# Kernel optimization log

Measured on AMD Instinct MI355X. Metric: run time of the kernel, lower is better.

The kernel has to match this reference:

```python
import jax, jax.numpy as jnp
import numpy as np

# plan steps: (downsample_factor, bins_min, bins_max)
PLAN = [(2, 10, 14), (4, 16, 20)]


def _downsample(x, scale):
    # F.interpolate(mode='linear', align_corners=False, scale_factor=1/scale)
    in_len = x.shape[-1]
    out_len = in_len // scale
    sf = in_len / out_len
    src = jnp.maximum((jnp.arange(out_len, dtype=jnp.float32) + 0.5) * sf - 0.5, 0.0)
    i0 = jnp.floor(src).astype(jnp.int32)
    w = src - i0
    i1 = jnp.minimum(i0 + 1, in_len - 1)
    return x[..., i0] * (1.0 - w) + x[..., i1] * w


def _groupshiftadd(x, g):
    # one FFA butterfly stage with group size g
    B, C, R, nc = x.shape
    xg = x.reshape(B, C, R // g, g, nc)
    i = np.arange(g)
    iA = i // 2
    iB = iA + g // 2
    Bs = (i + 1) // 2
    # roll(v, Bs): y[j] = v[(j - Bs) mod nc]; static gather indices
    col = (np.arange(nc)[None, :] - Bs[:, None]) % nc  # (g, nc)
    a = xg[:, :, :, iA, :]                     # (B,C,G,g,nc)
    b = xg[:, :, :, iB[:, None], col]          # (B,C,G,g,nc) shifted rows
    return (a + b).reshape(B, C, R, nc)


def _forward(x):
    std_dev = jnp.std(x, axis=2, ddof=1)  # torch .std(2) is unbiased
    outs = []
    for ds, bmin, bmax in PLAN:
        down = _downsample(x, ds)
        L = down.shape[-1]
        for bins in range(bmin, bmax):
            trunc = L % bins
            arr = down[:, :, :L - trunc] if trunc else down
            r = arr.reshape(arr.shape[0], arr.shape[1], -1, bins)
            ini_rows = r.shape[2]
            k = int(np.ceil(np.log2(ini_rows)))
            target_rows = 2 ** k
            add = target_rows - ini_rows
            if add:
                pad = jnp.zeros((r.shape[0], r.shape[1], add, bins), r.dtype)
                r = jnp.concatenate([r, pad], axis=2)
            y = r
            for stage in range(1, k + 1):
                y = _groupshiftadd(y, 2 ** stage)
            mx = y.max(axis=3)
            # torch.median returns lower middle element for even sizes
            med = jnp.sort(y, axis=3)[..., (bins - 1) // 2]
            snr = (mx - med) / std_dev[:, :, None] / np.sqrt(float(ini_rows))
            outs.append(snr)  # (B, C, target_rows)
    return jnp.concatenate(outs, axis=2)


def setup_inputs() -> dict:
    key = jax.random.key(0)
    x = jax.random.normal(key, (8, 4, 262144), dtype=jnp.float32)
    return {"x": x}


def reference(x):
    return _forward(x)
```

## Files before the change

kernel.cpp:

```cpp
#include <hip/hip_runtime.h>
#include <cmath>


constexpr int NSEQ    = 32;
constexpr int NLEN    = 262144;
constexpr int OUTROWS = 81920;
constexpr int STDCH   = 32;

constexpr int cilog2(int v) { int r = 0; while (v > 1) { v >>= 1; ++r; } return r; }

constexpr size_t SCROFF[8] = {0, 6291456, 12582912, 18874368,
                              27262976, 29360128, 31981568, 34603008};

__device__ __forceinline__ unsigned bf16rne(float f) {
    unsigned u = __float_as_uint(f);
    return (u + 0x7FFFu + ((u >> 16) & 1u)) >> 16;
}
__device__ __forceinline__ unsigned pk2(float lo, float hi) {
    return bf16rne(lo) | (bf16rne(hi) << 16);
}

__global__ __launch_bounds__(256)
void std_partial(const float* __restrict__ x, float2* __restrict__ part)
{
    const int seq = blockIdx.x, ch = blockIdx.y;
    constexpr int N4 = NLEN / 4 / STDCH;
    const float4* xp = reinterpret_cast<const float4*>(x + (size_t)seq * NLEN) + (size_t)ch * N4;
    float s = 0.f, s2 = 0.f;
    for (int i = threadIdx.x; i < N4; i += 256) {
        float4 v = xp[i];
        s  += (v.x + v.y) + (v.z + v.w);
        s2 += (v.x * v.x + v.y * v.y) + (v.z * v.z + v.w * v.w);
    }
    #pragma unroll
    for (int off = 32; off > 0; off >>= 1) {
        s  += __shfl_down(s, off, 64);
        s2 += __shfl_down(s2, off, 64);
    }
    __shared__ float2 ws[4];
    const int w = threadIdx.x >> 6, l = threadIdx.x & 63;
    if (l == 0) ws[w] = make_float2(s, s2);
    __syncthreads();
    if (threadIdx.x == 0) {
        float a = ws[0].x + ws[1].x + ws[2].x + ws[3].x;
        float b = ws[0].y + ws[1].y + ws[2].y + ws[3].y;
        part[seq * STDCH + ch] = make_float2(a, b);
    }
}

template<int BINS, int G, int H1, int LP>
__device__ __forceinline__
void stageIP(float* __restrict__ buf, int s)
{
    constexpr int CST = G + 4;
    constexpr int PAIRS = G / 2;
    const int t = threadIdx.x;
    const int pr  = t & (PAIRS - 1);
    const int chi = t >> LP;
    const int c0  = chi * H1;
    const int half = 1 << (s - 1);
    const int qp = pr & (half - 1);
    const int grpbase = (pr >> (s - 1)) << s;
    const int rA = grpbase + qp, rB = rA + half, ro = grpbase + 2 * qp;
    const int shift = qp % BINS;

    float ra[H1], rb[H1 + 1];
    #pragma unroll
    for (int i = 0; i < H1; ++i) {
        int cc = c0 + i; if (cc >= BINS) cc = BINS - 1;
        ra[i] = buf[cc * CST + rA];
    }
    int idx = c0 - shift - 1; if (idx < 0) idx += BINS;
    #pragma unroll
    for (int i = 0; i < H1 + 1; ++i) {
        rb[i] = buf[idx * CST + rB];
        ++idx; if (idx == BINS) idx = 0;
    }
    __syncthreads();
    #pragma unroll
    for (int i = 0; i < H1; ++i) {
        const int c = c0 + i;
        if (c < BINS) {
            float2 o; o.x = ra[i] + rb[i + 1]; o.y = ra[i] + rb[i];
            *reinterpret_cast<float2*>(&buf[c * CST + ro]) = o;
        }
    }
    __syncthreads();
}

template<int DS, int BINS, int K, int S0, int CPAD>
__device__ __forceinline__
void passA_body(float* __restrict__ buf, const float* __restrict__ xs,
                unsigned short* __restrict__ scrC, int R, int blk, int sl)
{
    constexpr int G     = 1 << S0;
    constexpr int M     = 1 << (K - S0);
    constexpr int CST   = G + 4;
    constexpr int PAIRS = G / 2;
    constexpr int LP    = cilog2(PAIRS);
    constexpr int CS1   = 512 / PAIRS;
    constexpr int H1    = (BINS + CS1 - 1) / CS1;
    const int t = threadIdx.x;

    const int fmax = max(0, min(G * BINS, R * BINS - blk * G * BINS));

    if constexpr (DS == 2) {
        const float4* src4 = reinterpret_cast<const float4*>(xs + 2 * (size_t)blk * G * BINS);
        constexpr int NF4 = G * BINS / 2;
        for (int i = t; i < NF4; i += 512) {
            const int f0 = 2 * i;
            if (f0 < fmax) {
                float4 v = src4[i];
                int lr = f0 / BINS, c = f0 - lr * BINS;
                buf[c * CST + lr] = 0.5f * (v.x + v.y);
                if (f0 + 1 < fmax) {
                    int c1 = c + 1, lr1 = lr;
                    if (c1 == BINS) { c1 = 0; ++lr1; }
                    buf[c1 * CST + lr1] = 0.5f * (v.z + v.w);
                }
            }
        }
    } else {
        const float4* src4 = reinterpret_cast<const float4*>(xs + 4 * (size_t)blk * G * BINS);
        constexpr int NF4 = G * BINS;
        for (int i = t; i < NF4; i += 512) {
            if (i < fmax) {
                float4 v = src4[i];
                int lr = i / BINS, c = i - lr * BINS;
                buf[c * CST + lr] = 0.5f * (v.y + v.z);
            }
        }
    }
    for (int f = fmax + t; f < G * BINS; f += 512) {
        int lr = f / BINS, c = f - lr * BINS;
        buf[c * CST + lr] = 0.f;
    }
    __syncthreads();

    for (int s = 1; s <= S0; ++s)
        stageIP<BINS, G, H1, LP>(buf, s);

    const float* fin = buf;
    if constexpr (G == 512) {
        const int lr = t;
        unsigned u[CPAD / 2];
        #pragma unroll
        for (int k = 0; k < CPAD / 2; ++k) {
            const int ca = 2 * k, cbn = 2 * k + 1;
            float fa = (ca < BINS)  ? fin[ca * CST + lr]  : 0.f;
            float fb = (cbn < BINS) ? fin[cbn * CST + lr] : 0.f;
            u[k] = pk2(fa, fb);
        }
        unsigned short* dst = scrC + ((size_t)(sl * M + blk) * G + lr) * CPAD;
        if constexpr (CPAD == 12) {
            uint2* d2 = reinterpret_cast<uint2*>(dst);
            d2[0] = make_uint2(u[0], u[1]);
            d2[1] = make_uint2(u[2], u[3]);
            d2[2] = make_uint2(u[4], u[5]);
        } else {
            uint4* d4 = reinterpret_cast<uint4*>(dst);
            d4[0] = make_uint4(u[0], u[1], u[2], u[3]);
            d4[1] = make_uint4(u[4], u[5], u[6], u[7]);
        }
    } else {
        const int lr = t & 255, chh = t >> 8;
        constexpr int CH = CPAD / 2;
        unsigned u[CH / 2];
        #pragma unroll
        for (int k = 0; k < CH / 2; ++k) {
            const int ca = chh * CH + 2 * k, cbn = ca + 1;
            float fa = (ca < BINS)  ? fin[ca * CST + lr]  : 0.f;
            float fb = (cbn < BINS) ? fin[cbn * CST + lr] : 0.f;
            u[k] = pk2(fa, fb);
        }
        unsigned short* dst = scrC + ((size_t)(sl * M + blk) * G + lr) * CPAD + chh * CH;
        if constexpr (CH == 8) {
            *reinterpret_cast<uint4*>(dst) = make_uint4(u[0], u[1], u[2], u[3]);
        } else {
            unsigned* d = reinterpret_cast<unsigned*>(dst);
            #pragma unroll
            for (int k = 0; k < CH / 2; ++k) d[k] = u[k];
        }
    }
}

__global__ __launch_bounds__(512, 8)
void passA_all(const float* __restrict__ x, unsigned short* __restrict__ scr)
{
    __shared__ float buf[13 * 516];
    const int b = blockIdx.x;
    if (b < 4096) {
        const int cfg = b >> 10, r = b & 1023, blk = r & 31, sl = r >> 5;
        const float* xs = x + (size_t)sl * NLEN;
        switch (cfg) {
            case 0: passA_body<2, 10, 14, 9, 12>(buf, xs, scr + SCROFF[0], 13107, blk, sl); break;
            case 1: passA_body<2, 11, 14, 9, 12>(buf, xs, scr + SCROFF[1], 11915, blk, sl); break;
            case 2: passA_body<2, 12, 14, 9, 12>(buf, xs, scr + SCROFF[2], 10922, blk, sl); break;
            default: passA_body<2, 13, 14, 9, 16>(buf, xs, scr + SCROFF[3], 10082, blk, sl); break;
        }
    } else {
        const int b2 = b - 4096;
        const int cfg = b2 >> 9, r = b2 & 511, blk = r & 15, sl = r >> 4;
        const float* xs = x + (size_t)sl * NLEN;
        switch (cfg) {
            case 0: passA_body<4, 16, 12, 8, 16>(buf, xs, scr + SCROFF[4], 4096, blk, sl); break;
            case 1: passA_body<4, 17, 12, 8, 20>(buf, xs, scr + SCROFF[5], 3855, blk, sl); break;
            case 2: passA_body<4, 18, 12, 8, 20>(buf, xs, scr + SCROFF[6], 3640, blk, sl); break;
            default: passA_body<4, 19, 12, 8, 20>(buf, xs, scr + SCROFF[7], 3449, blk, sl); break;
        }
    }
}

template<int BINS, int M, int CST, int HB, int LQ>
__device__ __forceinline__
void fusedB(float* __restrict__ zpg, int s, int p, int sub)
{
    constexpr int QUADS = M / 4;
    const int Q   = sub & (QUADS - 1);
    const int chi = sub >> LQ;
    const int c0  = chi * HB;
    const int h = 1 << (s - 1), S = 1 << s;
    const int q  = Q & (h - 1);
    const int G2 = (Q >> (s - 1)) << (s + 1);
    const int rA0 = G2 + q, rA1 = rA0 + h, rB0 = G2 + S + q, rB1 = rB0 + h;
    const int vo = G2 + 4 * q;
    auto mbf = [](int x, int B) { int r = x % B; return r < 0 ? r + B : r; };
    const int ba1 = mbf(c0 - q - p * h - 1, BINS);
    const int bb0 = mbf(c0 - 2 * q - p * S - 2, BINS);
    const int bb1 = mbf(c0 - 3 * q - p * (S + h) - 3, BINS);

    float fa0[HB], fa1[HB + 1], fb0[HB + 2], fb1[HB + 3];
    #pragma unroll
    for (int i = 0; i < HB; ++i) {
        int cc = c0 + i; if (cc >= BINS) cc = BINS - 1;
        fa0[i] = zpg[cc * CST + rA0];
    }
    int idx = ba1;
    #pragma unroll
    for (int i = 0; i < HB + 1; ++i) {
        fa1[i] = zpg[idx * CST + rA1];
        ++idx; if (idx == BINS) idx = 0;
    }
    idx = bb0;
    #pragma unroll
    for (int i = 0; i < HB + 2; ++i) {
        fb0[i] = zpg[idx * CST + rB0];
        ++idx; if (idx == BINS) idx = 0;
    }
    idx = bb1;
    #pragma unroll
    for (int i = 0; i < HB + 3; ++i) {
        fb1[i] = zpg[idx * CST + rB1];
        ++idx; if (idx == BINS) idx = 0;
    }
    __syncthreads();
    #pragma unroll
    for (int i2 = 0; i2 < HB; ++i2) {
        const int c = c0 + i2;
        if (c < BINS) {
            float u0 = fa0[i2] + fa1[i2 + 1];
            float u1 = fa0[i2] + fa1[i2];
            float v0c  = fb0[i2 + 2] + fb1[i2 + 3];
            float v0p  = fb0[i2 + 1] + fb1[i2 + 2];
            float v1p  = fb0[i2 + 1] + fb1[i2 + 1];
            float v1pp = fb0[i2]     + fb1[i2];
            float4 o; o.x = u0 + v0c; o.y = u0 + v0p; o.z = u1 + v1p; o.w = u1 + v1pp;
            *reinterpret_cast<float4*>(&zpg[c * CST + vo]) = o;
        }
    }
    __syncthreads();
}

template<int BINS, int M, int CST, int HSB, int LP>
__device__ __forceinline__
void singleB(float* __restrict__ zpg, int s, int p, int sub)
{
    constexpr int PAIRSB = M / 2;
    const int pr  = sub & (PAIRSB - 1);
    const int chi = sub >> LP;
    const int c0  = chi * HSB;
    const int half = 1 << (s - 1);
    const int qp = pr & (half - 1);
    const int grpbase = (pr >> (s - 1)) << s;
    const int rA = grpbase + qp, rB = rA + half, ro = grpbase + 2 * qp;
    const int shift = (qp + p * half) % BINS;

    float ra[HSB], rb[HSB + 1];
    #pragma unroll
    for (int i = 0; i < HSB; ++i) {
        int cc = c0 + i; if (cc >= BINS) cc = BINS - 1;
        ra[i] = zpg[cc * CST + rA];
    }
    int idx = c0 - shift - 1;
    idx %= BINS; if (idx < 0) idx += BINS;
    #pragma unroll
    for (int i = 0; i < HSB + 1; ++i) {
        rb[i] = zpg[idx * CST + rB];
        ++idx; if (idx == BINS) idx = 0;
    }
    __syncthreads();
    #pragma unroll
    for (int i2 = 0; i2 < HSB; ++i2) {
        const int c = c0 + i2;
        if (c < BINS) {
            float2 o; o.x = ra[i2] + rb[i2 + 1]; o.y = ra[i2] + rb[i2];
            *reinterpret_cast<float2*>(&zpg[c * CST + ro]) = o;
        }
    }
    __syncthreads();
}

template<int BINS, int K, int S0, int CPAD, int OUTOFF>
__device__ __forceinline__
void passB_body(float* __restrict__ zb, float* __restrict__ s_red,
                const unsigned short* __restrict__ scrC, const float2* __restrict__ part,
                float* __restrict__ out, int R, int p_base, int sl)
{
    constexpr int G    = 1 << S0;
    constexpr int M    = 1 << (K - S0);
    constexpr int TS   = K - S0;
    constexpr int P    = 16;
    constexpr int CST  = M + 4;
    constexpr int BCST = BINS * CST;
    constexpr int LQB  = cilog2(M / 4);
    constexpr int CHB  = 32 / (M / 4);
    constexpr int HB   = (BINS + CHB - 1) / CHB;
    constexpr int LPB  = cilog2(M / 2);
    constexpr int CSB  = 32 / (M / 2);
    constexpr int HSB  = (BINS + CSB - 1) / CSB;

    const int t = threadIdx.x;

    if (t < 64) {
        float s = 0.f, s2 = 0.f;
        if (t < 32) { float2 pp = part[sl * STDCH + t]; s = pp.x; s2 = pp.y; }
        #pragma unroll
        for (int off = 16; off > 0; off >>= 1) {
            s  += __shfl_down(s, off, 64);
            s2 += __shfl_down(s2, off, 64);
        }
        if (t == 0) {
            const float n = (float)NLEN;
            s_red[0] = rsqrtf((s2 - s * s / n) / (n - 1.f)) * rsqrtf((float)R);
        }
    }

    {
        constexpr int RUN = P * CPAD / 4;
        constexpr int TOT = M * RUN;
        const unsigned short* base = scrC + (size_t)sl * M * G * CPAD + (size_t)p_base * CPAD;
        for (int i = t; i < TOT; i += 512) {
            const int v = i / RUN, r = i - v * RUN;
            const uint2 d = *reinterpret_cast<const uint2*>(base + (size_t)v * G * CPAD + 4 * r);
            const int e0 = 4 * r;
            const int pl = e0 / CPAD, c = e0 - pl * CPAD;
            float* zp = zb + pl * BCST + v;
            if (c + 0 < BINS) zp[(c + 0) * CST] = __uint_as_float(d.x << 16);
            if (c + 1 < BINS) zp[(c + 1) * CST] = __uint_as_float(d.x & 0xFFFF0000u);
            if (c + 2 < BINS) zp[(c + 2) * CST] = __uint_as_float(d.y << 16);
            if (c + 3 < BINS) zp[(c + 3) * CST] = __uint_as_float(d.y & 0xFFFF0000u);
        }
    }
    __syncthreads();

    const int sub = t & 31, pg = t >> 5;
    const int p = p_base + pg;
    float* zpg = zb + pg * BCST;
    fusedB<BINS, M, CST, HB, LQB>(zpg, 1, p, sub);
    fusedB<BINS, M, CST, HB, LQB>(zpg, 3, p, sub);
    if constexpr (TS == 5) {
        singleB<BINS, M, CST, HSB, LPB>(zpg, 5, p, sub);
    }

    constexpr int ROWS = P * M;
    if (t < ROWS) {
        const int pg2 = t >> TS;
        const int v   = t & (M - 1);
        const float* z = zb + pg2 * BCST;
        float a[BINS];
        #pragma unroll
        for (int c = 0; c < BINS; ++c) a[c] = z[c * CST + v];
        float mx = a[0];
        #pragma unroll
        for (int c = 1; c < BINS; ++c) mx = fmaxf(mx, a[c]);
        constexpr int MIDX = (BINS - 1) / 2;
        #pragma unroll
        for (int i = 0; i <= MIDX; ++i) {
            #pragma unroll
            for (int j = i + 1; j < BINS; ++j) {
                float lo = fminf(a[i], a[j]);
                float hi = fmaxf(a[i], a[j]);
                a[i] = lo; a[j] = hi;
            }
        }
        out[(size_t)sl * OUTROWS + OUTOFF + (size_t)p_base * M + t] = (mx - a[MIDX]) * s_red[0];
    }
}

__global__ __launch_bounds__(512, 6)
void passB_all(const unsigned short* __restrict__ scr, const float2* __restrict__ part,
               float* __restrict__ out)
{
    __shared__ float zb[16 * 13 * 36];
    __shared__ float s_red[1];
    const int b = blockIdx.x;
    if (b < 4096) {
        const int cfg = b >> 10, r = b & 1023, pb = r & 31, sl = r >> 5;
        const int p_base = pb * 16;
        switch (cfg) {
            case 0: passB_body<10, 14, 9, 12, 0>    (zb, s_red, scr + SCROFF[0], part, out, 13107, p_base, sl); break;
            case 1: passB_body<11, 14, 9, 12, 16384>(zb, s_red, scr + SCROFF[1], part, out, 11915, p_base, sl); break;
            case 2: passB_body<12, 14, 9, 12, 32768>(zb, s_red, scr + SCROFF[2], part, out, 10922, p_base, sl); break;
            default: passB_body<13, 14, 9, 16, 49152>(zb, s_red, scr + SCROFF[3], part, out, 10082, p_base, sl); break;
        }
    } else {
        const int b2 = b - 4096;
        const int cfg = b2 >> 9, r = b2 & 511, pb = r & 15, sl = r >> 4;
        const int p_base = pb * 16;
        switch (cfg) {
            case 0: passB_body<16, 12, 8, 16, 65536>(zb, s_red, scr + SCROFF[4], part, out, 4096, p_base, sl); break;
            case 1: passB_body<17, 12, 8, 20, 69632>(zb, s_red, scr + SCROFF[5], part, out, 3855, p_base, sl); break;
            case 2: passB_body<18, 12, 8, 20, 73728>(zb, s_red, scr + SCROFF[6], part, out, 3640, p_base, sl); break;
            default: passB_body<19, 12, 8, 20, 77824>(zb, s_red, scr + SCROFF[7], part, out, 3449, p_base, sl); break;
        }
    }
}

extern "C" void kernel_launch(void* const* d_in, const int* in_sizes, int n_in,
                              void* d_out, int out_size, void* d_ws, size_t ws_size,
                              hipStream_t stream)
{
    (void)in_sizes; (void)n_in; (void)out_size; (void)ws_size;
    const float* x = (const float*)d_in[0];
    float* out  = (float*)d_out;
    float* wsf  = (float*)d_ws;
    float2* part = reinterpret_cast<float2*>(wsf + 64);
    unsigned short* scr = reinterpret_cast<unsigned short*>(wsf + 2176);

    hipLaunchKernelGGL(std_partial, dim3(NSEQ, STDCH), dim3(256), 0, stream, x, part);
    hipLaunchKernelGGL(passA_all, dim3(6144), dim3(512), 0, stream, x, scr);
    hipLaunchKernelGGL(passB_all, dim3(6144), dim3(512), 0, stream, scr, part, out);
}
```

Before: 156.6 us.

## Fuse pairs of FFA butterfly stages in shared memory with swizzled row layout

Replaces the one-stage-per-sync in-place butterfly loop in passA with fused radix-4 steps (stages 1-2, then 3-4, 5-6, 7-8), plus a separate stage 9 when the group is 512 rows. Each thread now handles a quad of rows and writes float4 results. Shared-memory row indices get an XOR swizzle to reduce bank conflicts. This roughly halves the barriers and shared-memory round trips. In exchange it raises register pressure, so the launch-bounds occupancy hint drops from 8 to 6 blocks.

```diff
diff --git a/kernel.cpp b/kernel.cpp
--- a/kernel.cpp
+++ b/kernel.cpp
@@ -19,6 +19,7 @@
 __device__ __forceinline__ unsigned pk2(float lo, float hi) {
     return bf16rne(lo) | (bf16rne(hi) << 16);
 }
+__device__ __forceinline__ int swz(int r) { return r ^ (((r >> 4) & 7) << 2); }
 
 __global__ __launch_bounds__(256)
 void std_partial(const float* __restrict__ x, float2* __restrict__ part)
@@ -48,32 +49,118 @@
     }
 }
 
-template<int BINS, int G, int H1, int LP>
-__device__ __forceinline__
-void stageIP(float* __restrict__ buf, int s)
+template<int BINS, int G, int HB>
+__device__ __forceinline__
+void fusedA1ip(float* __restrict__ buf, int Q, int c0)
 {
     constexpr int CST = G + 4;
-    constexpr int PAIRS = G / 2;
-    const int t = threadIdx.x;
-    const int pr  = t & (PAIRS - 1);
-    const int chi = t >> LP;
-    const int c0  = chi * H1;
-    const int half = 1 << (s - 1);
-    const int qp = pr & (half - 1);
-    const int grpbase = (pr >> (s - 1)) << s;
-    const int rA = grpbase + qp, rB = rA + half, ro = grpbase + 2 * qp;
-    const int shift = qp % BINS;
+    const int r4 = swz(4 * Q);
+    float4 ff[HB + 3];
+    #pragma unroll
+    for (int j = 0; j < HB + 3; ++j) {
+        int cc = c0 - 3 + j;
+        if (cc < 0) cc += BINS;
+        if (cc >= BINS) cc -= BINS;
+        ff[j] = *reinterpret_cast<const float4*>(&buf[cc * CST + r4]);
+    }
+    __syncthreads();
+    #pragma unroll
+    for (int i = 0; i < HB; ++i) {
+        const int c = c0 + i;
+        if (c < BINS) {
+            float4 f = ff[i + 3], fm1 = ff[i + 2], fm2 = ff[i + 1], fm3 = ff[i];
+            float u0 = f.x + f.y;
+            float u1 = f.x + fm1.y;
+            float4 o;
+            o.x = u0 + (f.z + f.w);
+            o.y = u0 + (fm1.z + fm1.w);
+            o.z = u1 + (fm1.z + fm2.w);
+            o.w = u1 + (fm2.z + fm3.w);
+            *reinterpret_cast<float4*>(&buf[c * CST + r4]) = o;
+        }
+    }
+    __syncthreads();
+}
+
+template<int BINS, int G, int HB>
+__device__ __forceinline__
+void fusedAip(float* __restrict__ buf, int s, int Q, int c0)
+{
+    constexpr int CST = G + 4;
+    const int h = 1 << (s - 1), S = 1 << s;
+    const int q  = Q & (h - 1);
+    const int G2 = (Q >> (s - 1)) << (s + 1);
+    const int rA0 = swz(G2 + q),     rA1 = swz(G2 + q + h);
+    const int rB0 = swz(G2 + S + q), rB1 = swz(G2 + S + q + h);
+    const int vo  = swz(G2 + 4 * q);
+    auto mbf = [](int x) { int r = x % BINS; return r < 0 ? r + BINS : r; };
+    const int ba1 = mbf(c0 - q - 1);
+    const int bb0 = mbf(c0 - 2 * q - 2);
+    const int bb1 = mbf(c0 - 3 * q - 3);
+
+    float fa0[HB], fa1[HB + 1], fb0[HB + 2], fb1[HB + 3];
+    #pragma unroll
+    for (int i = 0; i < HB; ++i) {
+        int cc = c0 + i; if (cc >= BINS) cc = BINS - 1;
+        fa0[i] = buf[cc * CST + rA0];
+    }
+    int idx = ba1;
+    #pragma unroll
+    for (int i = 0; i < HB + 1; ++i) {
+        fa1[i] = buf[idx * CST + rA1];
+        ++idx; if (idx == BINS) idx = 0;
+    }
+    idx = bb0;
+    #pragma unroll
+    for (int i = 0; i < HB + 2; ++i) {
+        fb0[i] = buf[idx * CST + rB0];
+        ++idx; if (idx == BINS) idx = 0;
+    }
+    idx = bb1;
+    #pragma unroll
+    for (int i = 0; i < HB + 3; ++i) {
+        fb1[i] = buf[idx * CST + rB1];
+        ++idx; if (idx == BINS) idx = 0;
+    }
+    __syncthreads();
+    #pragma unroll
+    for (int i = 0; i < HB; ++i) {
+        const int c = c0 + i;
+        if (c < BINS) {
+            float u0 = fa0[i] + fa1[i + 1];
+            float u1 = fa0[i] + fa1[i];
+            float v0c  = fb0[i + 2] + fb1[i + 3];
+            float v0p  = fb0[i + 1] + fb1[i + 2];
+            float v1p  = fb0[i + 1] + fb1[i + 1];
+            float v1pp = fb0[i]     + fb1[i];
+            float4 o; o.x = u0 + v0c; o.y = u0 + v0p; o.z = u1 + v1p; o.w = u1 + v1pp;
+            *reinterpret_cast<float4*>(&buf[c * CST + vo]) = o;
+        }
+    }
+    __syncthreads();
+}
+
+template<int BINS, int G, int H1>
+__device__ __forceinline__
+void stage9IP(float* __restrict__ buf, int pr, int c0)
+{
+    constexpr int CST = G + 4;
+    const int sA = swz(pr);
+    const int sB = sA + 256;
+    const int so = swz(2 * pr);
+    const int shift = pr % BINS;
 
     float ra[H1], rb[H1 + 1];
     #pragma unroll
     for (int i = 0; i < H1; ++i) {
         int cc = c0 + i; if (cc >= BINS) cc = BINS - 1;
-        ra[i] = buf[cc * CST + rA];
-    }
-    int idx = c0 - shift - 1; if (idx < 0) idx += BINS;
+        ra[i] = buf[cc * CST + sA];
+    }
+    int idx = c0 - shift - 1;
+    idx %= BINS; if (idx < 0) idx += BINS;
     #pragma unroll
     for (int i = 0; i < H1 + 1; ++i) {
-        rb[i] = buf[idx * CST + rB];
+        rb[i] = buf[idx * CST + sB];
         ++idx; if (idx == BINS) idx = 0;
     }
     __syncthreads();
@@ -82,7 +169,7 @@
         const int c = c0 + i;
         if (c < BINS) {
             float2 o; o.x = ra[i] + rb[i + 1]; o.y = ra[i] + rb[i];
-            *reinterpret_cast<float2*>(&buf[c * CST + ro]) = o;
+            *reinterpret_cast<float2*>(&buf[c * CST + so]) = o;
         }
     }
     __syncthreads();
@@ -96,9 +183,11 @@
     constexpr int G     = 1 << S0;
     constexpr int M     = 1 << (K - S0);
     constexpr int CST   = G + 4;
-    constexpr int PAIRS = G / 2;
-    constexpr int LP    = cilog2(PAIRS);
-    constexpr int CS1   = 512 / PAIRS;
+    constexpr int QUADS = G / 4;
+    constexpr int LQ    = cilog2(QUADS);
+    constexpr int CHB   = 512 / QUADS;
+    constexpr int HB    = (BINS + CHB - 1) / CHB;
+    constexpr int CS1   = 512 / (G / 2);
     constexpr int H1    = (BINS + CS1 - 1) / CS1;
     const int t = threadIdx.x;
 
@@ -112,11 +201,11 @@
             if (f0 < fmax) {
                 float4 v = src4[i];
                 int lr = f0 / BINS, c = f0 - lr * BINS;
-                buf[c * CST + lr] = 0.5f * (v.x + v.y);
+                buf[c * CST + swz(lr)] = 0.5f * (v.x + v.y);
                 if (f0 + 1 < fmax) {
                     int c1 = c + 1, lr1 = lr;
                     if (c1 == BINS) { c1 = 0; ++lr1; }
-                    buf[c1 * CST + lr1] = 0.5f * (v.z + v.w);
+                    buf[c1 * CST + swz(lr1)] = 0.5f * (v.z + v.w);
                 }
             }
         }
@@ -127,22 +216,33 @@
             if (i < fmax) {
                 float4 v = src4[i];
                 int lr = i / BINS, c = i - lr * BINS;
-                buf[c * CST + lr] = 0.5f * (v.y + v.z);
+                buf[c * CST + swz(lr)] = 0.5f * (v.y + v.z);
             }
         }
     }
     for (int f = fmax + t; f < G * BINS; f += 512) {
         int lr = f / BINS, c = f - lr * BINS;
-        buf[c * CST + lr] = 0.f;
-    }
-    __syncthreads();
-
-    for (int s = 1; s <= S0; ++s)
-        stageIP<BINS, G, H1, LP>(buf, s);
+        buf[c * CST + swz(lr)] = 0.f;
+    }
+    __syncthreads();
+
+    {
+        const int Q  = t & (QUADS - 1);
+        const int c0 = (t >> LQ) * HB;
+        fusedA1ip<BINS, G, HB>(buf, Q, c0);
+        fusedAip<BINS, G, HB>(buf, 3, Q, c0);
+        fusedAip<BINS, G, HB>(buf, 5, Q, c0);
+        fusedAip<BINS, G, HB>(buf, 7, Q, c0);
+    }
+    if constexpr (S0 == 9) {
+        const int pr  = t & (G / 2 - 1);
+        const int c01 = (t >> (S0 - 1)) * H1;
+        stage9IP<BINS, G, H1>(buf, pr, c01);
+    }
 
     const float* fin = buf;
     if constexpr (G == 512) {
-        const int lr = t;
+        const int lr = swz(t);
         unsigned u[CPAD / 2];
         #pragma unroll
         for (int k = 0; k < CPAD / 2; ++k) {
@@ -151,7 +251,7 @@
             float fb = (cbn < BINS) ? fin[cbn * CST + lr] : 0.f;
             u[k] = pk2(fa, fb);
         }
-        unsigned short* dst = scrC + ((size_t)(sl * M + blk) * G + lr) * CPAD;
+        unsigned short* dst = scrC + ((size_t)(sl * M + blk) * G + t) * CPAD;
         if constexpr (CPAD == 12) {
             uint2* d2 = reinterpret_cast<uint2*>(dst);
             d2[0] = make_uint2(u[0], u[1]);
@@ -163,7 +263,8 @@
             d4[1] = make_uint4(u[4], u[5], u[6], u[7]);
         }
     } else {
-        const int lr = t & 255, chh = t >> 8;
+        const int lrn = t & 255, chh = t >> 8;
+        const int lr = swz(lrn);
         constexpr int CH = CPAD / 2;
         unsigned u[CH / 2];
         #pragma unroll
@@ -173,7 +274,7 @@
             float fb = (cbn < BINS) ? fin[cbn * CST + lr] : 0.f;
             u[k] = pk2(fa, fb);
         }
-        unsigned short* dst = scrC + ((size_t)(sl * M + blk) * G + lr) * CPAD + chh * CH;
+        unsigned short* dst = scrC + ((size_t)(sl * M + blk) * G + lrn) * CPAD + chh * CH;
         if constexpr (CH == 8) {
             *reinterpret_cast<uint4*>(dst) = make_uint4(u[0], u[1], u[2], u[3]);
         } else {
@@ -184,7 +285,7 @@
     }
 }
 
-__global__ __launch_bounds__(512, 8)
+__global__ __launch_bounds__(512, 6)
 void passA_all(const float* __restrict__ x, unsigned short* __restrict__ scr)
 {
     __shared__ float buf[13 * 516];
```

New measurement: 143.8 us. -8.1%, faster.
